# Performance work log

Measured on AMD Instinct MI355X. Metric: run time of the kernel, lower is better.

## Reference

```python
import jax, jax.numpy as jnp
import numpy as np


def _cdist(x, y):
    # Euclidean pairwise distances, (N,D) x (M,D) -> (N,M)
    x2 = jnp.sum(x * x, axis=1, keepdims=True)          # (N,1)
    y2 = jnp.sum(y * y, axis=1, keepdims=True).T        # (1,M)
    sq = x2 + y2 - 2.0 * (x @ y.T)
    return jnp.sqrt(jnp.maximum(sq, 0.0))


def setup_inputs() -> dict:
    key = jax.random.key(0)
    k1, k2, k3, k4 = jax.random.split(key, 4)
    return {
        "pred_feat": jax.random.normal(k1, (8192, 6), dtype=jnp.float32),
        "pred_decoder": jax.random.normal(k2, (4096, 4), dtype=jnp.float32),
        "input_data": jax.random.normal(k3, (4096, 4), dtype=jnp.float32),
        "gt_data": jax.random.normal(k4, (32768, 6), dtype=jnp.float32),
    }


def _repulsion_loss(pred_points, alpha=100.0, margin=0.3):
    N = pred_points.shape[0]
    d = _cdist(pred_points, pred_points)                # (N,N)
    eye = jnp.eye(N, dtype=d.dtype)
    d_no_self = d + 1e6 * eye
    min_dist = jnp.min(d_no_self, axis=1)               # (N,)
    penalty = jax.nn.softplus(alpha * (margin - min_dist))
    return jnp.mean(penalty ** 2)


def reference(pred_feat, pred_decoder, input_data, gt_data):
    # train_decoder=False branch of CombinedCriterionAEImpulse.forward
    pred_points = pred_feat[:, :3]
    pred_normals = pred_feat[:, 3:]
    gt_points = gt_data[:, :3]
    gt_normals = gt_data[:, 3:]

    # nearest-neighbor matching: NxL cdist + argmin + gather
    dists = _cdist(pred_points, gt_points)              # (N,L)
    min_indices = jnp.argmin(dists, axis=1)             # (N,)
    closest_gt_points = gt_points[min_indices]          # (N,3)

    attraction_loss = jnp.mean((pred_points - closest_gt_points) ** 2)
    repulsion = _repulsion_loss(pred_points)
    inlier_loss = attraction_loss + repulsion

    # normal alignment loss
    closest_gt_normals = gt_normals[min_indices]        # (N,3)
    eps = 1e-05
    pn = pred_normals / jnp.maximum(
        jnp.linalg.norm(pred_normals, axis=1, keepdims=True), eps)
    gn = closest_gt_normals / jnp.maximum(
        jnp.linalg.norm(closest_gt_normals, axis=1, keepdims=True), eps)
    cos_theta = jnp.sum(pn * gn, axis=1)
    norm_loss = jnp.mean(1.0 - cos_theta)

    combined_loss = inlier_loss + norm_loss * 10.0
    return combined_loss
```

## Files before the change

kernel.cpp:

```cpp
#include <hip/hip_runtime.h>
#include <cstdint>

typedef unsigned short ushort_t;
typedef unsigned int u32;
typedef __attribute__((ext_vector_type(8))) short bf16x8;
typedef __attribute__((ext_vector_type(16))) float f32x16;

#define N_PRED 8192
#define N_GT   32768

#define NN_SPL 128
#define RP_SPL 32
#define NN_BLOCKS 2048
#define RP_BLOCKS 512

#define O_CRP  4194304u
#define O_PART 5242880u

__device__ __forceinline__ float max3f(float a, float b, float c) {
    float d;
    asm("v_max3_f32 %0, %1, %2, %3" : "=v"(d) : "v"(a), "v"(b), "v"(c));
    return d;
}
__device__ __forceinline__ ushort_t f2b(float v) {
    u32 b = __float_as_uint(v);
    return (ushort_t)((b + 0x7FFFu + ((b >> 16) & 1u)) >> 16);
}
__device__ __forceinline__ float b2f(ushort_t h) {
    return __uint_as_float((u32)h << 16);
}
__device__ __forceinline__ float red16(const f32x16 a, float best) {
    const float m0 = max3f(a[0], a[1], a[2]);
    const float m1 = max3f(a[3], a[4], a[5]);
    const float m2 = max3f(a[6], a[7], a[8]);
    const float m3 = max3f(a[9], a[10], a[11]);
    const float m4 = max3f(a[12], a[13], a[14]);
    const float m5 = max3f(m0, m1, a[15]);
    const float m6 = max3f(m2, m3, m4);
    return max3f(best, m5, m6);
}

#define MASKROW(ACC)                                               \
    {                                                              \
        _Pragma("unroll")                                          \
        for (int _r = 0; _r < 16; ++_r) {                          \
            const int _row = (_r & 3) + 8 * (_r >> 2) + rowoff;    \
            ACC[_r] = (_row == col) ? -3.0e38f : ACC[_r];          \
        }                                                          \
    }

template <bool DIAG>
__device__ __forceinline__ void scan8(const bf16x8* __restrict__ ap,
                                      const bf16x8 B0, const bf16x8 B1,
                                      const bf16x8 B2, const bf16x8 B3,
                                      const int ts0, const int ts1,
                                      const int ts2, const int ts3,
                                      const int col, const int rowoff,
                                      float& b0, float& b1, float& b2, float& b3) {
    const f32x16 zc = {};
    bf16x8 Acur = ap[0];
#pragma unroll
    for (int t = 0; t < 8; ++t) {
        const bf16x8 Anxt = (t < 7) ? ap[(t + 1) * 64] : Acur;
        f32x16 d0 = __builtin_amdgcn_mfma_f32_32x32x16_bf16(Acur, B0, zc, 0, 0, 0);
        f32x16 d1 = __builtin_amdgcn_mfma_f32_32x32x16_bf16(Acur, B1, zc, 0, 0, 0);
        if (DIAG && t == ts0) MASKROW(d0);
        b0 = red16(d0, b0);
        d0 = __builtin_amdgcn_mfma_f32_32x32x16_bf16(Acur, B2, zc, 0, 0, 0);
        if (DIAG && t == ts1) MASKROW(d1);
        b1 = red16(d1, b1);
        d1 = __builtin_amdgcn_mfma_f32_32x32x16_bf16(Acur, B3, zc, 0, 0, 0);
        if (DIAG && t == ts2) MASKROW(d0);
        b2 = red16(d0, b2);
        if (DIAG && t == ts3) MASKROW(d1);
        b3 = red16(d1, b3);
        Acur = Anxt;
    }
}

__global__ __launch_bounds__(256) void k_pair(const float* __restrict__ pred,
                                              const float* __restrict__ gt,
                                              float* __restrict__ chunkNN,
                                              float* __restrict__ chunkRP) {
    __shared__ bf16x8 As[512];
    const int w = threadIdx.x >> 6;
    const int lane = threadIdx.x & 63;
    const int b = blockIdx.x;
    const bool isNN = (b < NN_BLOCKS);
    const int pgBase = isNN ? (b >> 7) : ((b - NN_BLOCKS) >> 5);
    const int sp     = isNN ? (b & (NN_SPL - 1)) : ((b - NN_BLOCKS) & (RP_SPL - 1));
    const int pg = pgBase * 4 + w;

    const float* __restrict__ src = isNN ? gt : pred;
    {
        const int idx = threadIdx.x;
        const int gidx = sp * 256 + idx;
        const float x = src[gidx * 6 + 0], y = src[gidx * 6 + 1], z = src[gidx * 6 + 2];
        const ushort_t xh = f2b(x), yh = f2b(y), zh = f2b(z);
        const ushort_t xl = f2b(x - b2f(xh));
        const ushort_t yl = f2b(y - b2f(yh));
        const ushort_t zl = f2b(z - b2f(zh));
        const float wv = -0.5f * fmaf(z, z, fmaf(y, y, x * x));
        const ushort_t wh = f2b(wv);
        const ushort_t wl = f2b(wv - b2f(wh));
        bf16x8 h0, h1;
        h0[0] = (short)xh; h0[1] = (short)yh; h0[2] = (short)zh; h0[3] = (short)xh;
        h0[4] = (short)yh; h0[5] = (short)zh; h0[6] = (short)xl; h0[7] = (short)yl;
        h1[0] = (short)zl; h1[1] = (short)wh; h1[2] = (short)wl; h1[3] = 0;
        h1[4] = 0; h1[5] = 0; h1[6] = 0; h1[7] = 0;
        const int t = idx >> 5, row_ = idx & 31;
        As[t * 64 + row_] = h0;
        As[t * 64 + 32 + row_] = h1;
    }

    const int col = lane & 31;
    const int kh = lane >> 5;
    const int rowoff = kh * 4;
    const ushort_t ONE = 0x3F80;
    bf16x8 B[4];
#pragma unroll
    for (int j = 0; j < 4; ++j) {
        const int p = pg * 128 + j * 32 + col;
        const float x = pred[p * 6 + 0], y = pred[p * 6 + 1], z = pred[p * 6 + 2];
        const ushort_t xh = f2b(x), yh = f2b(y), zh = f2b(z);
        const ushort_t xl = f2b(x - b2f(xh));
        const ushort_t yl = f2b(y - b2f(yh));
        const ushort_t zl = f2b(z - b2f(zh));
        B[j][0] = (short)(kh ? zh : xh);
        B[j][1] = (short)(kh ? ONE : yh);
        B[j][2] = (short)(kh ? ONE : zh);
        B[j][3] = (short)(kh ? 0 : xl);
        B[j][4] = (short)(kh ? 0 : yl);
        B[j][5] = (short)(kh ? 0 : zl);
        B[j][6] = (short)(kh ? 0 : xh);
        B[j][7] = (short)(kh ? 0 : yh);
    }
    __syncthreads();

    const bf16x8* ap = &As[lane];
    float b0 = -3.0e38f, b1 = -3.0e38f, b2 = -3.0e38f, b3 = -3.0e38f;

    const bool diag = (!isNN) && (sp == (pg >> 1));
    if (diag) {
        const int tb = (w & 1) * 4;
        scan8<true>(ap, B[0], B[1], B[2], B[3], tb, tb + 1, tb + 2, tb + 3,
                    col, rowoff, b0, b1, b2, b3);
    } else {
        scan8<false>(ap, B[0], B[1], B[2], B[3], -1, -1, -1, -1,
                     col, rowoff, b0, b1, b2, b3);
    }

    b0 = fmaxf(b0, __shfl_xor(b0, 32));
    b1 = fmaxf(b1, __shfl_xor(b1, 32));
    b2 = fmaxf(b2, __shfl_xor(b2, 32));
    b3 = fmaxf(b3, __shfl_xor(b3, 32));

    if (lane < 32) {
        float* chunk = isNN ? chunkNN : chunkRP;
        const int base = sp * N_PRED + pg * 128 + col;
        chunk[base +  0] = b0;
        chunk[base + 32] = b1;
        chunk[base + 64] = b2;
        chunk[base + 96] = b3;
    }
}

__global__ __launch_bounds__(256) void k_fin(const float* __restrict__ pred,
                                             const float* __restrict__ gt,
                                             const float* __restrict__ chunkNN,
                                             const float* __restrict__ chunkRP,
                                             float* __restrict__ partials) {
    const int wave = threadIdx.x >> 6;
    const int lane = threadIdx.x & 63;
    const int p = blockIdx.x * 4 + wave;

    const float px = pred[p * 6 + 0], py = pred[p * 6 + 1], pz = pred[p * 6 + 2];

    float m = chunkNN[lane * N_PRED + p];
    int c = lane;
    {
        const float m1 = chunkNN[(lane + 64) * N_PRED + p];
        const bool tk = (m1 > m);
        m = tk ? m1 : m;
        c = tk ? (lane + 64) : c;
    }
#pragma unroll
    for (int off = 32; off > 0; off >>= 1) {
        const float om = __shfl_xor(m, off);
        const int   oc = __shfl_xor(c, off);
        const bool take = (om > m) || (om == m && oc < c);
        m = take ? om : m;
        c = take ? oc : c;
    }
    float bh = -3.0e38f;
    int bj = 0x7FFFFFFF;
#pragma unroll
    for (int i = 0; i < 4; ++i) {
        const int g = c * 256 + i * 64 + lane;
        const float x = gt[g * 6 + 0], y = gt[g * 6 + 1], z = gt[g * 6 + 2];
        const float w = -0.5f * fmaf(z, z, fmaf(y, y, x * x));
        const float h = fmaf(px, x, fmaf(py, y, fmaf(pz, z, w)));
        if (h > bh) { bh = h; bj = g; }
    }
#pragma unroll
    for (int off = 32; off > 0; off >>= 1) {
        const float oh = __shfl_xor(bh, off);
        const int og = __shfl_xor(bj, off);
        const bool take = (oh > bh) || (oh == bh && og < bj);
        bh = take ? oh : bh;
        bj = take ? og : bj;
    }
    const int j = bj;

    float rm = (lane < 32) ? chunkRP[lane * N_PRED + p] : -3.0e38f;
    int rc = (lane < 32) ? lane : 0;
#pragma unroll
    for (int off = 32; off > 0; off >>= 1) {
        const float om = __shfl_xor(rm, off);
        const int   oc = __shfl_xor(rc, off);
        const bool take = (om > rm) || (om == rm && oc < rc);
        rm = take ? om : rm;
        rc = take ? oc : rc;
    }
    float hr = -3.0e38f;
#pragma unroll
    for (int i = 0; i < 4; ++i) {
        const int q = rc * 256 + i * 64 + lane;
        const float x = pred[q * 6 + 0], y = pred[q * 6 + 1], z = pred[q * 6 + 2];
        const float w = -0.5f * fmaf(z, z, fmaf(y, y, x * x));
        float h = fmaf(px, x, fmaf(py, y, fmaf(pz, z, w)));
        h = (q == p) ? -3.0e38f : h;
        hr = fmaxf(hr, h);
    }
#pragma unroll
    for (int off = 32; off > 0; off >>= 1) hr = fmaxf(hr, __shfl_xor(hr, off));

    __shared__ float red[4][3];
    if (lane == 0) {
        const float gx = gt[j * 6 + 0], gy = gt[j * 6 + 1], gz = gt[j * 6 + 2];
        const float dx = px - gx, dy = py - gy, dz = pz - gz;
        const float att = dx * dx + dy * dy + dz * dz;

        const float pnx = pred[p * 6 + 3], pny = pred[p * 6 + 4], pnz = pred[p * 6 + 5];
        const float gnx = gt[j * 6 + 3],   gny = gt[j * 6 + 4],   gnz = gt[j * 6 + 5];
        const float pl = fmaxf(sqrtf(pnx * pnx + pny * pny + pnz * pnz), 1e-5f);
        const float gl = fmaxf(sqrtf(gnx * gnx + gny * gny + gnz * gnz), 1e-5f);
        const float nrm = 1.0f - (pnx * gnx + pny * gny + pnz * gnz) / (pl * gl);

        const float pp2 = px * px + py * py + pz * pz;
        float d2 = fmaf(-2.0f, hr, pp2);
        d2 = fmaxf(d2, 0.0f);
        const float xa = 100.0f * (0.3f - sqrtf(d2));
        const float sp2 = fmaxf(xa, 0.0f) + log1pf(expf(-fabsf(xa)));

        red[wave][0] = att;
        red[wave][1] = nrm;
        red[wave][2] = sp2 * sp2;
    }
    __syncthreads();
    if (threadIdx.x < 3)
        partials[blockIdx.x * 3 + threadIdx.x] =
            red[0][threadIdx.x] + red[1][threadIdx.x] +
            red[2][threadIdx.x] + red[3][threadIdx.x];
}

__device__ __forceinline__ float wave_reduce(float v) {
#pragma unroll
    for (int off = 32; off > 0; off >>= 1) v += __shfl_down(v, off, 64);
    return v;
}

__global__ __launch_bounds__(256) void k_comb(const float* __restrict__ partials,
                                              float* __restrict__ out) {
    float a = 0.f, n = 0.f, r = 0.f;
    const int t = threadIdx.x;
#pragma unroll
    for (int k = 0; k < 8; ++k) {
        const int row = t + k * 256;
        a += partials[row * 3 + 0];
        n += partials[row * 3 + 1];
        r += partials[row * 3 + 2];
    }
    a = wave_reduce(a);
    n = wave_reduce(n);
    r = wave_reduce(r);
    __shared__ float red[3][4];
    const int wave = t >> 6, lane = t & 63;
    if (lane == 0) { red[0][wave] = a; red[1][wave] = n; red[2][wave] = r; }
    __syncthreads();
    if (t == 0) {
        const float A = red[0][0] + red[0][1] + red[0][2] + red[0][3];
        const float Nn = red[1][0] + red[1][1] + red[1][2] + red[1][3];
        const float R = red[2][0] + red[2][1] + red[2][2] + red[2][3];
        out[0] = A / (float)(N_PRED * 3) + R / (float)N_PRED + 10.0f * (Nn / (float)N_PRED);
    }
}

extern "C" void kernel_launch(void* const* d_in, const int* in_sizes, int n_in,
                              void* d_out, int out_size, void* d_ws, size_t ws_size,
                              hipStream_t stream) {
    const float* pred = (const float*)d_in[0];
    const float* gt   = (const float*)d_in[3];
    float* out = (float*)d_out;
    char* ws = (char*)d_ws;

    float* chunkNN = (float*)ws;
    float* chunkRP = (float*)(ws + O_CRP);
    float* partials = (float*)(ws + O_PART);

    k_pair<<<NN_BLOCKS + RP_BLOCKS, 256, 0, stream>>>(pred, gt, chunkNN, chunkRP);
    k_fin<<<N_PRED / 4, 256, 0, stream>>>(pred, gt, chunkNN, chunkRP, partials);
    k_comb<<<1, 256, 0, stream>>>(partials, out);
}
```

Measured before the change: 41.31 us.

## Replace brute-force GT nearest-neighbor MFMA scan with z-binned sort and pruned search

Drops the dense pred-by-GT MFMA distance pass. GT points are now counting-sorted into z-bins across three kernels (count, scan, scatter), each sorted slab of 512 records its z range, and each prediction scans slabs nearest-first, stopping once the z-gap bound exceeds its best distance. The repulsion pass is retiled to 512-point chunks with 16 splits. This is meant to remove most of the O(N·L) NN work, at the cost of extra launches, atomics, data-dependent wave loops and a tie-break order that may differ from the reference in rare cases.

Result: slower. 143.8 us (+248.1%).

```diff
diff --git a/kernel.cpp b/kernel.cpp
--- a/kernel.cpp
+++ b/kernel.cpp
@@ -3,19 +3,27 @@
 
 typedef unsigned short ushort_t;
 typedef unsigned int u32;
+typedef unsigned long long u64;
+typedef __attribute__((ext_vector_type(4))) float v4f;
 typedef __attribute__((ext_vector_type(8))) short bf16x8;
 typedef __attribute__((ext_vector_type(16))) float f32x16;
 
 #define N_PRED 8192
 #define N_GT   32768
-
-#define NN_SPL 128
-#define RP_SPL 32
-#define NN_BLOCKS 2048
-#define RP_BLOCKS 512
-
-#define O_CRP  4194304u
-#define O_PART 5242880u
+#define NBIN   512
+#define NSPLIT 64
+#define MARGIN2 1e-5f
+
+#define RP_BLOCKS 256
+#define SCAT_BLOCKS 128
+
+#define O_SGTIDX 524288u
+#define O_COUNTS 655360u
+#define O_CURS   720896u
+#define O_LOU    722944u
+#define O_HIU    723200u
+#define O_CRP    786432u
+#define O_PART   1310720u
 
 __device__ __forceinline__ float max3f(float a, float b, float c) {
     float d;
@@ -26,8 +34,17 @@
     u32 b = __float_as_uint(v);
     return (ushort_t)((b + 0x7FFFu + ((b >> 16) & 1u)) >> 16);
 }
-__device__ __forceinline__ float b2f(ushort_t h) {
-    return __uint_as_float((u32)h << 16);
+__device__ __forceinline__ float b2f(ushort_t h) { return __uint_as_float((u32)h << 16); }
+__device__ __forceinline__ u32 packf(float v) {
+    const u32 b = __float_as_uint(v);
+    return b ^ ((u32)((int)b >> 31) | 0x80000000u);
+}
+__device__ __forceinline__ float unpackf(u32 u) {
+    return __uint_as_float((u >> 31) ? (u ^ 0x80000000u) : ~u);
+}
+__device__ __forceinline__ int zbin(float z) {
+    int b = (int)((z + 4.0f) * 64.0f);
+    return b < 0 ? 0 : (b > NBIN - 1 ? NBIN - 1 : b);
 }
 __device__ __forceinline__ float red16(const f32x16 a, float best) {
     const float m0 = max3f(a[0], a[1], a[2]);
@@ -39,7 +56,6 @@
     const float m6 = max3f(m2, m3, m4);
     return max3f(best, m5, m6);
 }
-
 #define MASKROW(ACC)                                               \
     {                                                              \
         _Pragma("unroll")                                          \
@@ -49,19 +65,57 @@
         }                                                          \
     }
 
+__global__ __launch_bounds__(256) void k_count(const float* __restrict__ gt,
+                                               u32* __restrict__ counts) {
+    __shared__ u32 h[NBIN];
+    const int tid = threadIdx.x;
+    h[tid] = 0; h[tid + 256] = 0;
+    __syncthreads();
+    const int base = blockIdx.x * 1024;
+#pragma unroll
+    for (int k = 0; k < 4; ++k) {
+        const int i = base + k * 256 + tid;
+        atomicAdd(&h[zbin(gt[i * 6 + 2])], 1u);
+    }
+    __syncthreads();
+    counts[blockIdx.x * NBIN + tid] = h[tid];
+    counts[blockIdx.x * NBIN + tid + 256] = h[tid + 256];
+}
+
+__global__ __launch_bounds__(512) void k_scan(const u32* __restrict__ counts,
+                                              u32* __restrict__ cursors,
+                                              u32* __restrict__ loU,
+                                              u32* __restrict__ hiU) {
+    __shared__ u32 tmp[NBIN];
+    const int tid = threadIdx.x;
+    u32 cnt = 0;
+#pragma unroll
+    for (int k = 0; k < 32; ++k) cnt += counts[k * NBIN + tid];
+    tmp[tid] = cnt;
+    __syncthreads();
+    for (int off = 1; off < NBIN; off <<= 1) {
+        u32 add = (tid >= off) ? tmp[tid - off] : 0u;
+        __syncthreads();
+        tmp[tid] += add;
+        __syncthreads();
+    }
+    cursors[tid] = tmp[tid] - cnt;
+    if (tid < NSPLIT) { loU[tid] = 0xFFFFFFFFu; hiU[tid] = 0u; }
+}
+
 template <bool DIAG>
-__device__ __forceinline__ void scan8(const bf16x8* __restrict__ ap,
-                                      const bf16x8 B0, const bf16x8 B1,
-                                      const bf16x8 B2, const bf16x8 B3,
-                                      const int ts0, const int ts1,
-                                      const int ts2, const int ts3,
-                                      const int col, const int rowoff,
-                                      float& b0, float& b1, float& b2, float& b3) {
+__device__ __forceinline__ void scan16(const bf16x8* __restrict__ ap,
+                                       const bf16x8 B0, const bf16x8 B1,
+                                       const bf16x8 B2, const bf16x8 B3,
+                                       const int ts0, const int ts1,
+                                       const int ts2, const int ts3,
+                                       const int col, const int rowoff,
+                                       float& b0, float& b1, float& b2, float& b3) {
     const f32x16 zc = {};
     bf16x8 Acur = ap[0];
 #pragma unroll
-    for (int t = 0; t < 8; ++t) {
-        const bf16x8 Anxt = (t < 7) ? ap[(t + 1) * 64] : Acur;
+    for (int t = 0; t < 16; ++t) {
+        const bf16x8 Anxt = (t < 15) ? ap[(t + 1) * 64] : Acur;
         f32x16 d0 = __builtin_amdgcn_mfma_f32_32x32x16_bf16(Acur, B0, zc, 0, 0, 0);
         f32x16 d1 = __builtin_amdgcn_mfma_f32_32x32x16_bf16(Acur, B1, zc, 0, 0, 0);
         if (DIAG && t == ts0) MASKROW(d0);
@@ -78,24 +132,43 @@
     }
 }
 
-__global__ __launch_bounds__(256) void k_pair(const float* __restrict__ pred,
-                                              const float* __restrict__ gt,
-                                              float* __restrict__ chunkNN,
-                                              float* __restrict__ chunkRP) {
-    __shared__ bf16x8 As[512];
+__global__ __launch_bounds__(256) void k_mid(const float* __restrict__ pred,
+                                             const float* __restrict__ gt,
+                                             u32* __restrict__ cursors,
+                                             v4f* __restrict__ sGt,
+                                             u32* __restrict__ sGtIdx,
+                                             u32* __restrict__ loU,
+                                             u32* __restrict__ hiU,
+                                             float* __restrict__ chunkRP) {
+    __shared__ bf16x8 As[1024];
+    const int b = blockIdx.x;
+    if (b < SCAT_BLOCKS) {
+        const int i = b * 256 + threadIdx.x;
+        const float x = gt[i * 6 + 0], y = gt[i * 6 + 1], z = gt[i * 6 + 2];
+        const u32 pos = atomicAdd(&cursors[zbin(z)], 1u);
+        v4f v;
+        v.x = x; v.y = y; v.z = z;
+        v.w = -0.5f * fmaf(z, z, fmaf(y, y, x * x));
+        sGt[pos] = v;
+        sGtIdx[pos] = (u32)i;
+        const int s = pos >> 9;
+        const u32 pz = packf(z);
+        atomicMin(&loU[s], pz);
+        atomicMax(&hiU[s], pz);
+        return;
+    }
+    const int rb = b - SCAT_BLOCKS;
     const int w = threadIdx.x >> 6;
     const int lane = threadIdx.x & 63;
-    const int b = blockIdx.x;
-    const bool isNN = (b < NN_BLOCKS);
-    const int pgBase = isNN ? (b >> 7) : ((b - NN_BLOCKS) >> 5);
-    const int sp     = isNN ? (b & (NN_SPL - 1)) : ((b - NN_BLOCKS) & (RP_SPL - 1));
+    const int pgBase = rb >> 4;
+    const int sp = rb & 15;
     const int pg = pgBase * 4 + w;
 
-    const float* __restrict__ src = isNN ? gt : pred;
-    {
-        const int idx = threadIdx.x;
-        const int gidx = sp * 256 + idx;
-        const float x = src[gidx * 6 + 0], y = src[gidx * 6 + 1], z = src[gidx * 6 + 2];
+#pragma unroll
+    for (int k = 0; k < 2; ++k) {
+        const int idx = k * 256 + threadIdx.x;
+        const int gidx = sp * 512 + idx;
+        const float x = pred[gidx * 6 + 0], y = pred[gidx * 6 + 1], z = pred[gidx * 6 + 2];
         const ushort_t xh = f2b(x), yh = f2b(y), zh = f2b(z);
         const ushort_t xl = f2b(x - b2f(xh));
         const ushort_t yl = f2b(y - b2f(yh));
@@ -139,35 +212,34 @@
 
     const bf16x8* ap = &As[lane];
     float b0 = -3.0e38f, b1 = -3.0e38f, b2 = -3.0e38f, b3 = -3.0e38f;
-
-    const bool diag = (!isNN) && (sp == (pg >> 1));
+    const bool diag = (sp == pgBase);
     if (diag) {
-        const int tb = (w & 1) * 4;
-        scan8<true>(ap, B[0], B[1], B[2], B[3], tb, tb + 1, tb + 2, tb + 3,
-                    col, rowoff, b0, b1, b2, b3);
+        const int tb = w * 4;
+        scan16<true>(ap, B[0], B[1], B[2], B[3], tb, tb + 1, tb + 2, tb + 3,
+                     col, rowoff, b0, b1, b2, b3);
     } else {
-        scan8<false>(ap, B[0], B[1], B[2], B[3], -1, -1, -1, -1,
-                     col, rowoff, b0, b1, b2, b3);
-    }
-
+        scan16<false>(ap, B[0], B[1], B[2], B[3], -1, -1, -1, -1,
+                      col, rowoff, b0, b1, b2, b3);
+    }
     b0 = fmaxf(b0, __shfl_xor(b0, 32));
     b1 = fmaxf(b1, __shfl_xor(b1, 32));
     b2 = fmaxf(b2, __shfl_xor(b2, 32));
     b3 = fmaxf(b3, __shfl_xor(b3, 32));
-
     if (lane < 32) {
-        float* chunk = isNN ? chunkNN : chunkRP;
         const int base = sp * N_PRED + pg * 128 + col;
-        chunk[base +  0] = b0;
-        chunk[base + 32] = b1;
-        chunk[base + 64] = b2;
-        chunk[base + 96] = b3;
+        chunkRP[base +  0] = b0;
+        chunkRP[base + 32] = b1;
+        chunkRP[base + 64] = b2;
+        chunkRP[base + 96] = b3;
     }
 }
 
 __global__ __launch_bounds__(256) void k_fin(const float* __restrict__ pred,
                                              const float* __restrict__ gt,
-                                             const float* __restrict__ chunkNN,
+                                             const v4f* __restrict__ sGt,
+                                             const u32* __restrict__ sGtIdx,
+                                             const u32* __restrict__ loU,
+                                             const u32* __restrict__ hiU,
                                              const float* __restrict__ chunkRP,
                                              float* __restrict__ partials) {
     const int wave = threadIdx.x >> 6;
@@ -175,57 +247,73 @@
     const int p = blockIdx.x * 4 + wave;
 
     const float px = pred[p * 6 + 0], py = pred[p * 6 + 1], pz = pred[p * 6 + 2];
-
-    float m = chunkNN[lane * N_PRED + p];
-    int c = lane;
-    {
-        const float m1 = chunkNN[(lane + 64) * N_PRED + p];
-        const bool tk = (m1 > m);
-        m = tk ? m1 : m;
-        c = tk ? (lane + 64) : c;
-    }
+    const float pp2 = px * px + py * py + pz * pz;
+
+    const float zlo = unpackf(loU[lane]);
+    const float zhi = unpackf(hiU[lane]);
+    const float gap = fmaxf(0.0f, fmaxf(zlo - pz, pz - zhi));
+    const float gap2 = gap * gap;
+
+    float mg = gap;
+    int mt = lane;
 #pragma unroll
     for (int off = 32; off > 0; off >>= 1) {
-        const float om = __shfl_xor(m, off);
-        const int   oc = __shfl_xor(c, off);
-        const bool take = (om > m) || (om == m && oc < c);
-        m = take ? om : m;
-        c = take ? oc : c;
-    }
+        const float og = __shfl_xor(mg, off);
+        const int ot = __shfl_xor(mt, off);
+        const bool take = (og < mg) || (og == mg && ot < mt);
+        mg = take ? og : mg;
+        mt = take ? ot : mt;
+    }
+
     float bh = -3.0e38f;
-    int bj = 0x7FFFFFFF;
-#pragma unroll
-    for (int i = 0; i < 4; ++i) {
-        const int g = c * 256 + i * 64 + lane;
-        const float x = gt[g * 6 + 0], y = gt[g * 6 + 1], z = gt[g * 6 + 2];
-        const float w = -0.5f * fmaf(z, z, fmaf(y, y, x * x));
-        const float h = fmaf(px, x, fmaf(py, y, fmaf(pz, z, w)));
-        if (h > bh) { bh = h; bj = g; }
+    int borig = 0x7FFFFFFF;
+    u64 scanned = 0ull;
+    int t = mt;
+    while (true) {
+#pragma unroll 2
+        for (int i = 0; i < 8; ++i) {
+            const int g = t * 512 + i * 64 + lane;
+            const v4f v = sGt[g];
+            const float h = fmaf(px, v.x, fmaf(py, v.y, fmaf(pz, v.z, v.w)));
+            const int orig = (int)sGtIdx[g];
+            const bool take = (h > bh) || (h == bh && orig < borig);
+            bh = take ? h : bh;
+            borig = take ? orig : borig;
+        }
+        scanned |= (1ull << t);
+        float hb = bh;
+#pragma unroll
+        for (int off = 32; off > 0; off >>= 1) hb = fmaxf(hb, __shfl_xor(hb, off));
+        const float d2ub = fmaxf(fmaf(-2.0f, hb, pp2), 0.0f);
+        const bool need = (gap2 <= d2ub + MARGIN2) && !((scanned >> lane) & 1ull);
+        const u64 mask = __ballot(need);
+        if (mask == 0ull) break;
+        t = __ffsll(mask) - 1;
     }
 #pragma unroll
     for (int off = 32; off > 0; off >>= 1) {
         const float oh = __shfl_xor(bh, off);
-        const int og = __shfl_xor(bj, off);
-        const bool take = (oh > bh) || (oh == bh && og < bj);
+        const int og = __shfl_xor(borig, off);
+        const bool take = (oh > bh) || (oh == bh && og < borig);
         bh = take ? oh : bh;
-        bj = take ? og : bj;
-    }
-    const int j = bj;
-
-    float rm = (lane < 32) ? chunkRP[lane * N_PRED + p] : -3.0e38f;
-    int rc = (lane < 32) ? lane : 0;
+        borig = take ? og : borig;
+    }
+    const int j = borig;
+
+    float rm = (lane < 16) ? chunkRP[lane * N_PRED + p] : -3.0e38f;
+    int rc = (lane < 16) ? lane : 0;
 #pragma unroll
     for (int off = 32; off > 0; off >>= 1) {
         const float om = __shfl_xor(rm, off);
-        const int   oc = __shfl_xor(rc, off);
+        const int oc = __shfl_xor(rc, off);
         const bool take = (om > rm) || (om == rm && oc < rc);
         rm = take ? om : rm;
         rc = take ? oc : rc;
     }
     float hr = -3.0e38f;
-#pragma unroll
-    for (int i = 0; i < 4; ++i) {
-        const int q = rc * 256 + i * 64 + lane;
+#pragma unroll 2
+    for (int i = 0; i < 8; ++i) {
+        const int q = rc * 512 + i * 64 + lane;
         const float x = pred[q * 6 + 0], y = pred[q * 6 + 1], z = pred[q * 6 + 2];
         const float w = -0.5f * fmaf(z, z, fmaf(y, y, x * x));
         float h = fmaf(px, x, fmaf(py, y, fmaf(pz, z, w)));
@@ -247,7 +335,6 @@
         const float gl = fmaxf(sqrtf(gnx * gnx + gny * gny + gnz * gnz), 1e-5f);
         const float nrm = 1.0f - (pnx * gnx + pny * gny + pnz * gnz) / (pl * gl);
 
-        const float pp2 = px * px + py * py + pz * pz;
         float d2 = fmaf(-2.0f, hr, pp2);
         d2 = fmaxf(d2, 0.0f);
         const float xa = 100.0f * (0.3f - sqrtf(d2));
@@ -304,11 +391,20 @@
     float* out = (float*)d_out;
     char* ws = (char*)d_ws;
 
-    float* chunkNN = (float*)ws;
+    v4f* sGt      = (v4f*)ws;
+    u32* sGtIdx   = (u32*)(ws + O_SGTIDX);
+    u32* counts   = (u32*)(ws + O_COUNTS);
+    u32* cursors  = (u32*)(ws + O_CURS);
+    u32* loU      = (u32*)(ws + O_LOU);
+    u32* hiU      = (u32*)(ws + O_HIU);
     float* chunkRP = (float*)(ws + O_CRP);
     float* partials = (float*)(ws + O_PART);
 
-    k_pair<<<NN_BLOCKS + RP_BLOCKS, 256, 0, stream>>>(pred, gt, chunkNN, chunkRP);
-    k_fin<<<N_PRED / 4, 256, 0, stream>>>(pred, gt, chunkNN, chunkRP, partials);
+    k_count<<<32, 256, 0, stream>>>(gt, counts);
+    k_scan<<<1, 512, 0, stream>>>(counts, cursors, loU, hiU);
+    k_mid<<<SCAT_BLOCKS + RP_BLOCKS, 256, 0, stream>>>(pred, gt, cursors, sGt, sGtIdx,
+                                                       loU, hiU, chunkRP);
+    k_fin<<<N_PRED / 4, 256, 0, stream>>>(pred, gt, sGt, sGtIdx, loU, hiU,
+                                          chunkRP, partials);
     k_comb<<<1, 256, 0, stream>>>(partials, out);
 }
```
